# Optimization experiments

Hardware: AMD Instinct MI355X
Metric: run time of the kernel (lower is better)

Reference implementation:

```python
import jax, jax.numpy as jnp
import numpy as np

N, C, H, W, Z = 2, 12, 128, 128, 128
SMOOTH = 1e-5  # MONAI DiceLoss smooth_nr / smooth_dr defaults
BETA = 3.0


def setup_inputs() -> dict:
    key = jax.random.key(0)
    k1, k2, k3 = jax.random.split(key, 3)
    inp = jax.random.normal(k1, (N, C, H, W, Z), dtype=jnp.float32)
    tgt = jax.random.randint(k2, (N, 1, H, W, Z), 0, C, dtype=jnp.int64)
    mat = jax.random.uniform(k3, (C, C), dtype=jnp.float32)
    return {"input": inp, "target": tgt, "matrix_penalty": mat}


def reference(input, target, matrix_penalty):
    c = input.shape[1]
    tgt = target[:, 0]  # (n,h,w,z) integer labels

    # ---- CE part of DiceCELoss (softmax cross-entropy, mean reduction) ----
    logp = jax.nn.log_softmax(input, axis=1)            # (n,c,h,w,z)
    ce = -jnp.mean(jnp.take_along_axis(logp, target, axis=1))

    # ---- Dice part (to_onehot_y=True, softmax=True, include_background) ----
    p = jnp.exp(logp)                                    # softmax probs
    t1h = jax.nn.one_hot(tgt, c, axis=1, dtype=p.dtype)  # (n,c,h,w,z)
    axes = (2, 3, 4)                                     # reduce spatial dims
    inter = jnp.sum(t1h * p, axis=axes)                  # (n,c)
    ground_o = jnp.sum(t1h, axis=axes)
    pred_o = jnp.sum(p, axis=axes)
    dice = jnp.mean(1.0 - (2.0 * inter + SMOOTH) / (ground_o + pred_o + SMOOTH))

    # ---- DOMINO penalty: mean over pixels of M[t,:] . softmax(logits) ----
    rows = matrix_penalty[tgt]                           # (n,h,w,z,c) gather
    p_last = jnp.moveaxis(p, 1, -1)                      # (n,h,w,z,c)
    penalty = BETA * jnp.mean(jnp.sum(rows * p_last, axis=-1))

    return ce + dice + penalty
```

## Files before the change

### kernel.cpp

```cpp
#include <hip/hip_runtime.h>

#define HWZ (128*128*128)
#define NN 2
#define CC 12
#define BLOCK 256
#define TV 256
#define TILES (HWZ / TV)
#define BX 768
#define NREP 8

static constexpr float SMOOTHF = 1e-5f;
static constexpr float BETAF   = 3.0f;

#define GLD16(gsrc, ldst) __builtin_amdgcn_global_load_lds( \
  (const __attribute__((address_space(1))) void*)(gsrc),    \
  (__attribute__((address_space(3))) void*)(ldst), 16, 0, 0)


__global__ __launch_bounds__(BLOCK) void loss_main(
    const float* __restrict__ in, const int* __restrict__ tgt,
    const float* __restrict__ mat, float* __restrict__ ws)
{
    __shared__ __align__(16) float lds_in[2][CC][TV];
    __shared__ __align__(16) float smat[CC * CC];
    __shared__ float red[4][38];

    const int tid  = threadIdx.x;
    const int wave = tid >> 6;
    const int lane = tid & 63;
    if (tid < CC * CC) smat[tid] = mat[tid];

    const int n = blockIdx.y;
    const float* __restrict__ inb = in + (size_t)n * CC * HWZ;
    const int*   __restrict__ tb  = tgt + (size_t)n * HWZ;

    float ce = 0.f, pen = 0.f;
    float inter[CC], pred[CC];
    unsigned long long cnt_pack = 0ull;
    #pragma unroll
    for (int c = 0; c < CC; ++c) { inter[c] = 0.f; pred[c] = 0.f; }

    __syncthreads();

    int tile = blockIdx.x;
    int p = 0;
    int tcur = 0;
    {
        const int v0 = tile * TV;
        #pragma unroll
        for (int k = 0; k < 3; ++k) {
            const int c = wave * 3 + k;
            GLD16(inb + (size_t)c * HWZ + v0 + lane * 4, &lds_in[0][c][lane * 4]);
        }
        tcur = tb[v0 + tid];
    }

    #pragma unroll 1
    for (; tile < TILES; tile += BX) {
        const int nxt = tile + BX;
        int tnext = 0;
        if (nxt < TILES) {
            const int v0n = nxt * TV;
            #pragma unroll
            for (int k = 0; k < 3; ++k) {
                const int c = wave * 3 + k;
                GLD16(inb + (size_t)c * HWZ + v0n + lane * 4, &lds_in[p ^ 1][c][lane * 4]);
            }
            tnext = tb[v0n + tid];
            asm volatile("s_waitcnt vmcnt(4)" ::: "memory");
        } else {
            asm volatile("s_waitcnt vmcnt(0)" ::: "memory");
        }
        __builtin_amdgcn_s_barrier();

        const float* lbuf = &lds_in[p][0][0];
        const int t = tcur;

        float e[CC], xt = 0.f, sum = 0.f;
        #pragma unroll
        for (int c = 0; c < CC; ++c) {
            const float x = lbuf[c * TV + tid];
            xt = (c == t) ? x : xt;
            e[c] = __expf(x);
            sum += e[c];
        }
        const float inv = __builtin_amdgcn_rcpf(sum);
        const float lse = __logf(sum);

        float rw[CC];
        *reinterpret_cast<float4*>(&rw[0]) = *reinterpret_cast<const float4*>(&smat[t * CC + 0]);
        *reinterpret_cast<float4*>(&rw[4]) = *reinterpret_cast<const float4*>(&smat[t * CC + 4]);
        *reinterpret_cast<float4*>(&rw[8]) = *reinterpret_cast<const float4*>(&smat[t * CC + 8]);

        float pdot = 0.f;
        #pragma unroll
        for (int c = 0; c < CC; ++c) {
            const float pr = e[c] * inv;
            pred[c]  += pr;
            inter[c] += (c == t) ? pr : 0.f;
            pdot += rw[c] * pr;
        }
        ce  += lse - xt;
        pen += pdot;
        cnt_pack += 1ull << (t * 4);

        __builtin_amdgcn_s_barrier();
        p ^= 1;
        tcur = tnext;
    }

    float acc[38];
    acc[0] = ce; acc[1] = pen;
    #pragma unroll
    for (int c = 0; c < CC; ++c) {
        acc[2 + c]  = inter[c];
        acc[14 + c] = pred[c];
        acc[26 + c] = (float)((cnt_pack >> (c * 4)) & 15ull);
    }

    #pragma unroll
    for (int k = 0; k < 38; ++k) {
        float v = acc[k];
        #pragma unroll
        for (int off = 32; off >= 1; off >>= 1)
            v += __shfl_xor(v, off, 64);
        if (lane == 0) red[wave][k] = v;
    }
    __syncthreads();

    if (tid < 38) {
        const float s4 = red[0][tid] + red[1][tid] + red[2][tid] + red[3][tid];
        int gidx;
        if (tid < 2)       gidx = tid;
        else if (tid < 14) gidx = 2  + n * CC + (tid - 2);
        else if (tid < 26) gidx = 26 + n * CC + (tid - 14);
        else               gidx = 50 + n * CC + (tid - 26);
        const int r = blockIdx.x & (NREP - 1);
        atomicAdd(&ws[r * 74 + gidx], s4);
    }
}

__global__ void loss_final(const float* __restrict__ ws, float* __restrict__ out)
{
    __shared__ float agg[74];
    const int tid = threadIdx.x;
    if (tid < 74) {
        float s = 0.f;
        #pragma unroll
        for (int r = 0; r < NREP; ++r) s += ws[r * 74 + tid];
        agg[tid] = s;
    }
    __syncthreads();
    if (tid == 0) {
        const float V = (float)((long)NN * HWZ);
        const float ce  = agg[0] / V;
        const float pen = BETAF * agg[1] / V;
        float dice = 0.f;
        for (int i = 0; i < NN * CC; ++i) {
            const float it = agg[2 + i], pr = agg[26 + i], ct = agg[50 + i];
            dice += 1.f - (2.f * it + SMOOTHF) / (ct + pr + SMOOTHF);
        }
        dice *= (1.0f / (NN * CC));
        out[0] = ce + dice + pen;
    }
}

extern "C" void kernel_launch(void* const* d_in, const int* in_sizes, int n_in,
                              void* d_out, int out_size, void* d_ws, size_t ws_size,
                              hipStream_t stream)
{
    const float* in  = (const float*)d_in[0];
    const int*   tgt = (const int*)d_in[1];
    const float* mat = (const float*)d_in[2];
    float* ws  = (float*)d_ws;
    float* out = (float*)d_out;

    hipMemsetAsync(ws, 0, NREP * 74 * sizeof(float), stream);
    dim3 grid(BX, NN);
    loss_main<<<grid, BLOCK, 0, stream>>>(in, tgt, mat, ws);
    loss_final<<<1, 128, 0, stream>>>(ws, out);
}
```

Before: 68.51 us.

## Deepen prefetch to a 4-slot LDS ring and stage targets through LDS

Replaces the two-buffer scheme with a four-slot LDS ring that keeps three tiles in flight. Targets are now loaded asynchronously into LDS by one wave instead of through registers, and the trailing barrier in each iteration is dropped. The grid is halved so each block streams more tiles, and the per-class count packing widens to 5 bits to hold the larger per-thread counts. The aim is more bytes in flight to hide HBM latency, at the cost of more LDS per block and hand-tuned vmcnt waits that must match the exact number of issued loads.

```diff
diff --git a/kernel.cpp b/kernel.cpp
--- a/kernel.cpp
+++ b/kernel.cpp
@@ -6,7 +6,8 @@
 #define BLOCK 256
 #define TV 256
 #define TILES (HWZ / TV)
-#define BX 768
+#define BX 384
+#define RING 4
 #define NREP 8
 
 static constexpr float SMOOTHF = 1e-5f;
@@ -21,7 +22,8 @@
     const float* __restrict__ in, const int* __restrict__ tgt,
     const float* __restrict__ mat, float* __restrict__ ws)
 {
-    __shared__ __align__(16) float lds_in[2][CC][TV];
+    __shared__ __align__(16) float lds_in[RING][CC][TV];
+    __shared__ __align__(16) int   lds_tg[RING][TV];
     __shared__ __align__(16) float smat[CC * CC];
     __shared__ float red[4][38];
 
@@ -29,10 +31,14 @@
     const int wave = tid >> 6;
     const int lane = tid & 63;
     if (tid < CC * CC) smat[tid] = mat[tid];
+    __syncthreads();
 
     const int n = blockIdx.y;
     const float* __restrict__ inb = in + (size_t)n * CC * HWZ;
     const int*   __restrict__ tb  = tgt + (size_t)n * HWZ;
+
+    const int start  = blockIdx.x;
+    const int ntiles = (TILES - 1 - start) / BX + 1;
 
     float ce = 0.f, pen = 0.f;
     float inter[CC], pred[CC];
@@ -40,46 +46,45 @@
     #pragma unroll
     for (int c = 0; c < CC; ++c) { inter[c] = 0.f; pred[c] = 0.f; }
 
-    __syncthreads();
-
-    int tile = blockIdx.x;
-    int p = 0;
-    int tcur = 0;
-    {
-        const int v0 = tile * TV;
+    auto STAGE = [&](int i) {
+        const int slot = i & (RING - 1);
+        const size_t v0 = (size_t)(start + i * BX) * TV;
         #pragma unroll
         for (int k = 0; k < 3; ++k) {
             const int c = wave * 3 + k;
-            GLD16(inb + (size_t)c * HWZ + v0 + lane * 4, &lds_in[0][c][lane * 4]);
+            GLD16(inb + (size_t)c * HWZ + v0 + lane * 4, &lds_in[slot][c][0]);
         }
-        tcur = tb[v0 + tid];
-    }
+        if (wave == 3) GLD16(tb + v0 + lane * 4, &lds_tg[slot][0]);
+    };
+
+    if (0 < ntiles) STAGE(0);
+    if (1 < ntiles) STAGE(1);
+    if (2 < ntiles) STAGE(2);
 
     #pragma unroll 1
-    for (; tile < TILES; tile += BX) {
-        const int nxt = tile + BX;
-        int tnext = 0;
-        if (nxt < TILES) {
-            const int v0n = nxt * TV;
-            #pragma unroll
-            for (int k = 0; k < 3; ++k) {
-                const int c = wave * 3 + k;
-                GLD16(inb + (size_t)c * HWZ + v0n + lane * 4, &lds_in[p ^ 1][c][lane * 4]);
-            }
-            tnext = tb[v0n + tid];
-            asm volatile("s_waitcnt vmcnt(4)" ::: "memory");
+    for (int i = 0; i < ntiles; ++i) {
+        const int beyond = (ntiles - 1 - i) > 2 ? 2 : (ntiles - 1 - i);
+        if (wave == 3) {
+            if      (beyond == 2) asm volatile("s_waitcnt vmcnt(8)" ::: "memory");
+            else if (beyond == 1) asm volatile("s_waitcnt vmcnt(4)" ::: "memory");
+            else                  asm volatile("s_waitcnt vmcnt(0)" ::: "memory");
         } else {
-            asm volatile("s_waitcnt vmcnt(0)" ::: "memory");
+            if      (beyond == 2) asm volatile("s_waitcnt vmcnt(6)" ::: "memory");
+            else if (beyond == 1) asm volatile("s_waitcnt vmcnt(3)" ::: "memory");
+            else                  asm volatile("s_waitcnt vmcnt(0)" ::: "memory");
         }
         __builtin_amdgcn_s_barrier();
+        asm volatile("" ::: "memory");
 
-        const float* lbuf = &lds_in[p][0][0];
-        const int t = tcur;
+        if (i + 3 < ntiles) STAGE(i + 3);
+
+        const int slot = i & (RING - 1);
+        const int t = lds_tg[slot][tid];
 
         float e[CC], xt = 0.f, sum = 0.f;
         #pragma unroll
         for (int c = 0; c < CC; ++c) {
-            const float x = lbuf[c * TV + tid];
+            const float x = lds_in[slot][c][tid];
             xt = (c == t) ? x : xt;
             e[c] = __expf(x);
             sum += e[c];
@@ -102,11 +107,7 @@
         }
         ce  += lse - xt;
         pen += pdot;
-        cnt_pack += 1ull << (t * 4);
-
-        __builtin_amdgcn_s_barrier();
-        p ^= 1;
-        tcur = tnext;
+        cnt_pack += 1ull << (t * 5);
     }
 
     float acc[38];
@@ -115,7 +116,7 @@
     for (int c = 0; c < CC; ++c) {
         acc[2 + c]  = inter[c];
         acc[14 + c] = pred[c];
-        acc[26 + c] = (float)((cnt_pack >> (c * 4)) & 15ull);
+        acc[26 + c] = (float)((cnt_pack >> (c * 5)) & 31ull);
     }
 
     #pragma unroll
```

New measurement: 73.61 us. 1.07x slower.
